# Optimization experiments

Measured on AMD Instinct MI355X. Metric: run time of the kernel, lower is better.

## Reference

```python
import jax, jax.numpy as jnp
import numpy as np

DIM = 64
NUM_HEADS = 2
HEAD_DIM = DIM // NUM_HEADS


def setup_inputs() -> dict:
    key = jax.random.key(0)
    k1, k2, k3 = jax.random.split(key, 3)
    b, c, h, w = 8, DIM, 256, 256
    x = jax.random.normal(k1, (b, c, h, w), dtype=jnp.float32)
    # 1x1 conv weights, stored as [out_ch, in_ch] (kernel spatial dims are 1)
    qkv_w = jax.random.normal(k2, (3 * c, c), dtype=jnp.float32) * (1.0 / np.sqrt(c))
    proj_w = jax.random.normal(k3, (c, c), dtype=jnp.float32) * (1.0 / np.sqrt(c))
    return {"x": x, "qkv_w": qkv_w, "proj_w": proj_w}


def _phi(t):
    # elu(x) + 1 feature map (positive-valued kernel features)
    return jax.nn.elu(t) + 1.0


def reference(x, qkv_w, proj_w):
    b, c, h, w = x.shape
    n = h * w
    # 1x1 conv == per-pixel channel matmul
    qkv = jnp.einsum('oc,bchw->bohw', qkv_w, x)  # [b, 3c, h, w]
    q, k, v = jnp.split(qkv, 3, axis=1)

    def reshape(t):
        return t.reshape(b, NUM_HEADS, HEAD_DIM, n)  # bhcn

    q_phi = _phi(reshape(q))
    k_phi = _phi(reshape(k))
    v_h = reshape(v)
    # KV outer product over the sequence dim: tiny [b, h, c, d]
    KV = jnp.einsum('bhcn,bhdn->bhcd', k_phi, v_h)
    out_h = jnp.einsum('bhcn,bhcd->bhdn', q_phi, KV)  # [b, h, d, n]
    out = out_h.reshape(b, c, h, w)
    return jnp.einsum('oc,bchw->bohw', proj_w, out)
```

## Files before the change

kernel.cpp:

```cpp
#include <hip/hip_runtime.h>
#include <hip/hip_bf16.h>

#define BATCH 8
#define CH    64
#define NPIX  65536
#define NHEAD 2
#define HDIM  32
#define P1_BLOCKS 32

typedef __attribute__((ext_vector_type(8))) short bf16x8;
typedef __attribute__((ext_vector_type(4))) float f32x4;

#define MFMA(a, b, c) __builtin_amdgcn_mfma_f32_16x16x32_bf16(a, b, c, 0, 0, 0)

__device__ __forceinline__ unsigned rne_pk(float lo, float hi) {
    unsigned ua = __float_as_uint(lo); ua += 0x7fffu + ((ua >> 16) & 1u);
    unsigned ub = __float_as_uint(hi); ub += 0x7fffu + ((ub >> 16) & 1u);
    return (ua >> 16) | (ub & 0xffff0000u);
}

__device__ __forceinline__ bf16x8 pack8(const float* f) {
    int4 iv;
    iv.x = (int)rne_pk(f[0], f[1]);
    iv.y = (int)rne_pk(f[2], f[3]);
    iv.z = (int)rne_pk(f[4], f[5]);
    iv.w = (int)rne_pk(f[6], f[7]);
    return *reinterpret_cast<bf16x8*>(&iv);
}

__device__ __forceinline__ float phi_f(float t) {
    return t > 0.0f ? t + 1.0f : __expf(t);
}

__device__ __forceinline__ bf16x8 load_w_frag(const float* W, int r0, int k0, int lane) {
    const float* p = W + (size_t)(r0 + (lane & 15)) * 64 + k0 + ((lane >> 4) << 3);
    float f[8];
    #pragma unroll
    for (int e = 0; e < 8; e++) f[e] = p[e];
    return pack8(f);
}

__global__ __launch_bounds__(256) void la_pass1(
    const float* __restrict__ x, const float* __restrict__ qkv_w,
    float* __restrict__ partials)
{
    __shared__ __align__(16) unsigned char smem[40960];

    const int tid  = threadIdx.x;
    const int lane = tid & 63;
    const int wv   = __builtin_amdgcn_readfirstlane(tid >> 6);
    const int b    = blockIdx.y;
    const int g    = lane >> 4;
    const int li   = lane & 15;

    unsigned short* kls = (unsigned short*)(smem + wv * 10240);
    unsigned short* vls = kls + 64 * 40;

    bf16x8 Wf[8][2];
    #pragma unroll
    for (int j = 0; j < 8; j++)
        #pragma unroll
        for (int ks = 0; ks < 2; ks++)
            Wf[j][ks] = load_w_frag(qkv_w, 64 + 16 * j, 32 * ks, lane);

    f32x4 kvacc[2][2][2];
    #pragma unroll
    for (int h = 0; h < 2; h++)
        #pragma unroll
        for (int mt = 0; mt < 2; mt++)
            #pragma unroll
            for (int nt = 0; nt < 2; nt++)
                kvacc[h][mt][nt] = (f32x4){0.f, 0.f, 0.f, 0.f};

    const float* xb = x + (size_t)b * CH * NPIX;

    for (int s = blockIdx.x * 4 + wv; s < 2048; s += P1_BLOCKS * 4) {
        const int px0 = s * 32;

        bf16x8 xa[2][2];
        #pragma unroll
        for (int mt = 0; mt < 2; mt++) {
            const float* xp = xb + px0 + 16 * mt + li;
            #pragma unroll
            for (int ks = 0; ks < 2; ks++) {
                float f[8];
                #pragma unroll
                for (int e = 0; e < 8; e++)
                    f[e] = xp[(size_t)(32 * ks + 8 * g + e) * NPIX];
                xa[mt][ks] = pack8(f);
            }
        }

        #pragma unroll
        for (int j = 0; j < 8; j++) {
            unsigned short* dst = (j < 4) ? kls : vls;
            const int crow = (j & 3) * 16 + li;
            #pragma unroll
            for (int mt = 0; mt < 2; mt++) {
                f32x4 acc = (f32x4){0.f, 0.f, 0.f, 0.f};
                acc = MFMA(xa[mt][0], Wf[j][0], acc);
                acc = MFMA(xa[mt][1], Wf[j][1], acc);
                float v0 = acc[0], v1 = acc[1], v2 = acc[2], v3 = acc[3];
                if (j < 4) { v0 = phi_f(v0); v1 = phi_f(v1); v2 = phi_f(v2); v3 = phi_f(v3); }
                *reinterpret_cast<uint2*>(dst + crow * 40 + 16 * mt + 4 * g) =
                    make_uint2(rne_pk(v0, v1), rne_pk(v2, v3));
            }
        }

        #pragma unroll
        for (int h = 0; h < 2; h++) {
            bf16x8 af[2], bv[2];
            #pragma unroll
            for (int mt = 0; mt < 2; mt++)
                af[mt] = *reinterpret_cast<const bf16x8*>(kls + (32 * h + 16 * mt + li) * 40 + 8 * g);
            #pragma unroll
            for (int nt = 0; nt < 2; nt++)
                bv[nt] = *reinterpret_cast<const bf16x8*>(vls + (32 * h + 16 * nt + li) * 40 + 8 * g);
            #pragma unroll
            for (int mt = 0; mt < 2; mt++)
                #pragma unroll
                for (int nt = 0; nt < 2; nt++)
                    kvacc[h][mt][nt] = MFMA(af[mt], bv[nt], kvacc[h][mt][nt]);
        }
    }

    __syncthreads();
    float* rbuf = (float*)smem;
    #pragma unroll
    for (int h = 0; h < 2; h++)
        #pragma unroll
        for (int mt = 0; mt < 2; mt++)
            #pragma unroll
            for (int nt = 0; nt < 2; nt++) {
                const int t = (h * 2 + mt) * 2 + nt;
                #pragma unroll
                for (int r = 0; r < 4; r++)
                    rbuf[wv * 2048 + t * 256 + (4 * g + r) * 16 + li] = kvacc[h][mt][nt][r];
            }
    __syncthreads();

    float* outp = partials + ((size_t)b * P1_BLOCKS + blockIdx.x) * 2048;
    for (int i = 0; i < 8; i++) {
        const int idx = i * 256 + tid;
        const float sum = rbuf[idx] + rbuf[2048 + idx] + rbuf[4096 + idx] + rbuf[6144 + idx];
        const int t = idx >> 8, within = idx & 255;
        const int row = within >> 4, col = within & 15;
        const int h = t >> 2, mt = (t >> 1) & 1, nt = t & 1;
        outp[(h * 32 + 16 * mt + row) * 32 + 16 * nt + col] = sum;
    }
}

__global__ __launch_bounds__(256) void la_reduce(
    const float* __restrict__ partials, float* __restrict__ kv)
{
    const int b = blockIdx.x;
    const int t = threadIdx.x;
    for (int e = t; e < 2048; e += 256) {
        const float* p = partials + (size_t)b * P1_BLOCKS * 2048 + e;
        float s = 0.0f;
        #pragma unroll
        for (int j = 0; j < P1_BLOCKS; j++) s += p[(size_t)j * 2048];
        kv[(size_t)b * 2048 + e] = s;
    }
}

__global__ __launch_bounds__(256) void la_pass2(
    const float* __restrict__ x, const float* __restrict__ qkv_w,
    const float* __restrict__ proj_w, const float* __restrict__ kv,
    float* __restrict__ y)
{
    __shared__ __align__(16) unsigned short sm2[4][2][16][72];

    const int tid  = threadIdx.x;
    const int lane = tid & 63;
    const int wv   = __builtin_amdgcn_readfirstlane(tid >> 6);
    const int b    = blockIdx.y;
    const int g    = lane >> 4;
    const int li   = lane & 15;

    unsigned short* qT = &sm2[wv][0][0][0];
    unsigned short* oT = &sm2[wv][1][0][0];

    bf16x8 Aq[4][2], Ap[4][2], Akv[2][2];
    #pragma unroll
    for (int mt = 0; mt < 4; mt++)
        #pragma unroll
        for (int ks = 0; ks < 2; ks++) {
            Aq[mt][ks] = load_w_frag(qkv_w, 16 * mt, 32 * ks, lane);
            Ap[mt][ks] = load_w_frag(proj_w, 16 * mt, 32 * ks, lane);
        }
    const float* kvb = kv + (size_t)b * NHEAD * HDIM * HDIM;
    #pragma unroll
    for (int h = 0; h < 2; h++)
        #pragma unroll
        for (int mtd = 0; mtd < 2; mtd++) {
            float f[8];
            #pragma unroll
            for (int e = 0; e < 8; e++)
                f[e] = kvb[h * 1024 + (8 * g + e) * 32 + 16 * mtd + li];
            Akv[h][mtd] = pack8(f);
        }

    const float* xb = x + (size_t)b * CH * NPIX;
    float*       yb = y + (size_t)b * CH * NPIX;

    for (int s = blockIdx.x * 4 + wv; s < 4096; s += 512) {
        const int px0 = s * 16;

        bf16x8 bx[2];
        const float* xp = xb + px0 + li;
        #pragma unroll
        for (int ks = 0; ks < 2; ks++) {
            float f[8];
            #pragma unroll
            for (int e = 0; e < 8; e++)
                f[e] = xp[(size_t)(32 * ks + 8 * g + e) * NPIX];
            bx[ks] = pack8(f);
        }

        #pragma unroll
        for (int mt = 0; mt < 4; mt++) {
            f32x4 acc = (f32x4){0.f, 0.f, 0.f, 0.f};
            acc = MFMA(Aq[mt][0], bx[0], acc);
            acc = MFMA(Aq[mt][1], bx[1], acc);
            const float p0 = phi_f(acc[0]), p1 = phi_f(acc[1]);
            const float p2 = phi_f(acc[2]), p3 = phi_f(acc[3]);
            *reinterpret_cast<uint2*>(qT + li * 72 + 16 * mt + 4 * g) =
                make_uint2(rne_pk(p0, p1), rne_pk(p2, p3));
        }

        #pragma unroll
        for (int h = 0; h < 2; h++) {
            const bf16x8 bq = *reinterpret_cast<const bf16x8*>(qT + li * 72 + 32 * h + 8 * g);
            #pragma unroll
            for (int mtd = 0; mtd < 2; mtd++) {
                f32x4 acc = (f32x4){0.f, 0.f, 0.f, 0.f};
                acc = MFMA(Akv[h][mtd], bq, acc);
                *reinterpret_cast<uint2*>(oT + li * 72 + 32 * h + 16 * mtd + 4 * g) =
                    make_uint2(rne_pk(acc[0], acc[1]), rne_pk(acc[2], acc[3]));
            }
        }

        const bf16x8 bo0 = *reinterpret_cast<const bf16x8*>(oT + li * 72 + 8 * g);
        const bf16x8 bo1 = *reinterpret_cast<const bf16x8*>(oT + li * 72 + 32 + 8 * g);
        #pragma unroll
        for (int mt = 0; mt < 4; mt++) {
            f32x4 acc = (f32x4){0.f, 0.f, 0.f, 0.f};
            acc = MFMA(Ap[mt][0], bo0, acc);
            acc = MFMA(Ap[mt][1], bo1, acc);
            #pragma unroll
            for (int r = 0; r < 4; r++)
                yb[(size_t)(16 * mt + 4 * g + r) * NPIX + px0 + li] = acc[r];
        }
    }
}

extern "C" void kernel_launch(void* const* d_in, const int* in_sizes, int n_in,
                              void* d_out, int out_size, void* d_ws, size_t ws_size,
                              hipStream_t stream) {
    (void)in_sizes; (void)n_in; (void)out_size; (void)ws_size;
    const float* x      = (const float*)d_in[0];
    const float* qkv_w  = (const float*)d_in[1];
    const float* proj_w = (const float*)d_in[2];
    float* yout = (float*)d_out;

    float* partials = (float*)d_ws;
    float* kv       = partials + (size_t)BATCH * P1_BLOCKS * 2048;

    la_pass1 <<<dim3(P1_BLOCKS, BATCH), dim3(256), 0, stream>>>(x, qkv_w, partials);
    la_reduce<<<dim3(BATCH),            dim3(256), 0, stream>>>(partials, kv);
    la_pass2 <<<dim3(128, BATCH),       dim3(256), 0, stream>>>(x, qkv_w, proj_w, kv, yout);
}
```

Baseline: 119.2 us.

## Prefetch next x tile in registers and widen grids for pass1, reduce, pass2

Both passes now load the next iteration's x tile into registers before computing the current one. The loops are fully unrolled to a fixed 4 iterations per wave, with more blocks launched (P1_BLOCKS 32→128, pass2 grid 128→256). The reduce kernel is spread over 64 blocks with four independent accumulators. The goal is to hide global load latency and raise occupancy and parallelism, at the cost of more registers and a larger partials buffer to reduce.

```diff
diff --git a/kernel.cpp b/kernel.cpp
--- a/kernel.cpp
+++ b/kernel.cpp
@@ -6,7 +6,7 @@
 #define NPIX  65536
 #define NHEAD 2
 #define HDIM  32
-#define P1_BLOCKS 32
+#define P1_BLOCKS 128
 
 typedef __attribute__((ext_vector_type(8))) short bf16x8;
 typedef __attribute__((ext_vector_type(4))) float f32x4;
@@ -73,21 +73,38 @@
                 kvacc[h][mt][nt] = (f32x4){0.f, 0.f, 0.f, 0.f};
 
     const float* xb = x + (size_t)b * CH * NPIX;
-
-    for (int s = blockIdx.x * 4 + wv; s < 2048; s += P1_BLOCKS * 4) {
-        const int px0 = s * 32;
-
+    const int s0 = blockIdx.x * 4 + wv;
+
+    float fr[2][2][8];
+    #pragma unroll
+    for (int mt = 0; mt < 2; mt++) {
+        const float* xp = xb + s0 * 32 + 16 * mt + li;
+        #pragma unroll
+        for (int ks = 0; ks < 2; ks++)
+            #pragma unroll
+            for (int e = 0; e < 8; e++)
+                fr[mt][ks][e] = xp[(size_t)(32 * ks + 8 * g + e) * NPIX];
+    }
+
+    #pragma unroll
+    for (int it = 0; it < 4; it++) {
         bf16x8 xa[2][2];
         #pragma unroll
-        for (int mt = 0; mt < 2; mt++) {
-            const float* xp = xb + px0 + 16 * mt + li;
-            #pragma unroll
-            for (int ks = 0; ks < 2; ks++) {
-                float f[8];
+        for (int mt = 0; mt < 2; mt++)
+            #pragma unroll
+            for (int ks = 0; ks < 2; ks++)
+                xa[mt][ks] = pack8(fr[mt][ks]);
+
+        if (it < 3) {
+            const int sn = s0 + (it + 1) * (P1_BLOCKS * 4);
+            #pragma unroll
+            for (int mt = 0; mt < 2; mt++) {
+                const float* xp = xb + sn * 32 + 16 * mt + li;
                 #pragma unroll
-                for (int e = 0; e < 8; e++)
-                    f[e] = xp[(size_t)(32 * ks + 8 * g + e) * NPIX];
-                xa[mt][ks] = pack8(f);
+                for (int ks = 0; ks < 2; ks++)
+                    #pragma unroll
+                    for (int e = 0; e < 8; e++)
+                        fr[mt][ks][e] = xp[(size_t)(32 * ks + 8 * g + e) * NPIX];
             }
         }
 
@@ -140,6 +157,7 @@
     __syncthreads();
 
     float* outp = partials + ((size_t)b * P1_BLOCKS + blockIdx.x) * 2048;
+    #pragma unroll
     for (int i = 0; i < 8; i++) {
         const int idx = i * 256 + tid;
         const float sum = rbuf[idx] + rbuf[2048 + idx] + rbuf[4096 + idx] + rbuf[6144 + idx];
@@ -153,15 +171,18 @@
 __global__ __launch_bounds__(256) void la_reduce(
     const float* __restrict__ partials, float* __restrict__ kv)
 {
-    const int b = blockIdx.x;
-    const int t = threadIdx.x;
-    for (int e = t; e < 2048; e += 256) {
-        const float* p = partials + (size_t)b * P1_BLOCKS * 2048 + e;
-        float s = 0.0f;
-        #pragma unroll
-        for (int j = 0; j < P1_BLOCKS; j++) s += p[(size_t)j * 2048];
-        kv[(size_t)b * 2048 + e] = s;
-    }
+    const int b = blockIdx.x >> 3;
+    const int e = (blockIdx.x & 7) * 256 + threadIdx.x;
+    const float* p = partials + (size_t)b * P1_BLOCKS * 2048 + e;
+    float s0 = 0.f, s1 = 0.f, s2 = 0.f, s3 = 0.f;
+    #pragma unroll 8
+    for (int j = 0; j < P1_BLOCKS; j += 4) {
+        s0 += p[(size_t)j * 2048];
+        s1 += p[(size_t)(j + 1) * 2048];
+        s2 += p[(size_t)(j + 2) * 2048];
+        s3 += p[(size_t)(j + 3) * 2048];
+    }
+    kv[(size_t)b * 2048 + e] = (s0 + s1) + (s2 + s3);
 }
 
 __global__ __launch_bounds__(256) void la_pass2(
@@ -204,18 +225,32 @@
     const float* xb = x + (size_t)b * CH * NPIX;
     float*       yb = y + (size_t)b * CH * NPIX;
 
-    for (int s = blockIdx.x * 4 + wv; s < 4096; s += 512) {
-        const int px0 = s * 16;
+    const int s0 = blockIdx.x * 4 + wv;
+    float fr[2][8];
+    {
+        const float* xp = xb + s0 * 16 + li;
+        #pragma unroll
+        for (int ks = 0; ks < 2; ks++)
+            #pragma unroll
+            for (int e = 0; e < 8; e++)
+                fr[ks][e] = xp[(size_t)(32 * ks + 8 * g + e) * NPIX];
+    }
+
+    #pragma unroll
+    for (int it = 0; it < 4; it++) {
+        const int px0 = (s0 + it * 1024) * 16;
 
         bf16x8 bx[2];
-        const float* xp = xb + px0 + li;
-        #pragma unroll
-        for (int ks = 0; ks < 2; ks++) {
-            float f[8];
-            #pragma unroll
-            for (int e = 0; e < 8; e++)
-                f[e] = xp[(size_t)(32 * ks + 8 * g + e) * NPIX];
-            bx[ks] = pack8(f);
+        #pragma unroll
+        for (int ks = 0; ks < 2; ks++) bx[ks] = pack8(fr[ks]);
+
+        if (it < 3) {
+            const float* xp = xb + (s0 + (it + 1) * 1024) * 16 + li;
+            #pragma unroll
+            for (int ks = 0; ks < 2; ks++)
+                #pragma unroll
+                for (int e = 0; e < 8; e++)
+                    fr[ks][e] = xp[(size_t)(32 * ks + 8 * g + e) * NPIX];
         }
 
         #pragma unroll
@@ -268,6 +303,6 @@
     float* kv       = partials + (size_t)BATCH * P1_BLOCKS * 2048;
 
     la_pass1 <<<dim3(P1_BLOCKS, BATCH), dim3(256), 0, stream>>>(x, qkv_w, partials);
-    la_reduce<<<dim3(BATCH),            dim3(256), 0, stream>>>(partials, kv);
-    la_pass2 <<<dim3(128, BATCH),       dim3(256), 0, stream>>>(x, qkv_w, proj_w, kv, yout);
-}
+    la_reduce<<<dim3(64),               dim3(256), 0, stream>>>(partials, kv);
+    la_pass2 <<<dim3(256, BATCH),       dim3(256), 0, stream>>>(x, qkv_w, proj_w, kv, yout);
+}
```

New measurement: 120.3 us. Within noise of the previous version (+0.9%).
